# Kernel tuning notes

Hardware: AMD Instinct MI355X
Metric: run time of the kernel (lower is better)

The kernel has to match this reference:

```python
import jax, jax.numpy as jnp
import numpy as np

DS_DIM = 2
N_EXPERTS = 64
N_CLASSES = 26
IMG = 68
BATCH = 8192
FLAT = 1960  # 10 * 14 * 14 after two conv+pool stages


def _conv2d(x, w, b):
    # x: [B, Cin, H, W], w: [Cout, Cin, kh, kw]
    y = jax.lax.conv_general_dilated(
        x, w, window_strides=(1, 1), padding='VALID',
        dimension_numbers=('NCHW', 'OIHW', 'NCHW'))
    return y + b[None, :, None, None]


def _maxpool2(x):
    return jax.lax.reduce_window(
        x, -jnp.inf, jax.lax.max,
        window_dimensions=(1, 1, 2, 2), window_strides=(1, 1, 2, 2),
        padding='VALID')


def setup_inputs() -> dict:
    key = jax.random.key(0)
    ks = jax.random.split(key, 14)
    x = jax.random.normal(ks[0], (BATCH, DS_DIM), dtype=jnp.float32)
    cls_idx = jax.random.randint(ks[1], (BATCH,), 0, N_CLASSES)
    images = jax.random.normal(ks[2], (N_CLASSES, 1, IMG, IMG), dtype=jnp.float32)
    s = 0.05
    conv1_w = jax.random.normal(ks[3], (5, 1, 5, 5), dtype=jnp.float32) * s
    conv1_b = jax.random.normal(ks[4], (5,), dtype=jnp.float32) * s
    conv2_w = jax.random.normal(ks[5], (10, 5, 5, 5), dtype=jnp.float32) * s
    conv2_b = jax.random.normal(ks[6], (10,), dtype=jnp.float32) * s
    fc1_w = jax.random.normal(ks[7], (500, FLAT + DS_DIM), dtype=jnp.float32) * s
    fc1_b = jax.random.normal(ks[8], (500,), dtype=jnp.float32) * s
    fc2_w = jax.random.normal(ks[9], (N_EXPERTS, 500), dtype=jnp.float32) * s
    fc2_b = jax.random.normal(ks[10], (N_EXPERTS,), dtype=jnp.float32) * s
    # geotorch-constrained expert matrices: B_A positive-semidefinite, C_A skew
    raw_b = jax.random.normal(ks[11], (N_EXPERTS, DS_DIM, DS_DIM), dtype=jnp.float32)
    A_B = jnp.einsum('nik,njk->nij', raw_b, raw_b) * 0.1        # PSD
    raw_c = jax.random.normal(ks[12], (N_EXPERTS, DS_DIM, DS_DIM), dtype=jnp.float32)
    A_C = (raw_c - jnp.swapaxes(raw_c, -1, -2)) * 0.5            # skew
    x_tar = jax.random.normal(ks[13], (1, DS_DIM), dtype=jnp.float32)
    return {'x': x, 'cls_idx': cls_idx, 'images': images,
            'conv1_w': conv1_w, 'conv1_b': conv1_b,
            'conv2_w': conv2_w, 'conv2_b': conv2_b,
            'fc1_w': fc1_w, 'fc1_b': fc1_b,
            'fc2_w': fc2_w, 'fc2_b': fc2_b,
            'A_B': A_B, 'A_C': A_C, 'x_tar': x_tar}


def reference(x, cls_idx, images, conv1_w, conv1_b, conv2_w, conv2_b,
              fc1_w, fc1_b, fc2_w, fc2_b, A_B, A_C, x_tar):
    # gating CNN: gather per-sample image by class index
    img = images[cls_idx]                             # [B, 1, 68, 68]
    h = _maxpool2(jax.nn.relu(_conv2d(img, conv1_w, conv1_b)))   # [B, 5, 32, 32]
    h = _maxpool2(jax.nn.relu(_conv2d(h, conv2_w, conv2_b)))     # [B, 10, 14, 14]
    h = h.reshape(h.shape[0], -1)                     # [B, 1960]
    h = jnp.concatenate([h, x], axis=1)               # [B, 1962]
    h = jax.nn.relu(h @ fc1_w.T + fc1_b)              # [B, 500]
    w_all = jax.nn.softmax(h @ fc2_w.T + fc2_b, axis=1)  # [B, N]
    # fused expert weighted-sum (original: python loop over N tiny matmuls)
    A = A_B + A_C                                     # [N, d, d]
    diff = x_tar - x                                  # [B, d]
    s_all = jnp.einsum('bn,nij,bj->bi', w_all, A, diff)
    return s_all
```

## Files before the change

### kernel.cpp

```cpp
#include <hip/hip_runtime.h>

#define WS_SC1    0
#define WS_FEAT   133120
#define WS_FC1P   184080
#define WS_W2     197080
#define WS_AFLAT  229848
#define WS_WX     230104

__global__ __launch_bounds__(256) void k_conv1(
    const float* __restrict__ images, const float* __restrict__ c1w,
    const float* __restrict__ c1b, const float* __restrict__ fc2w,
    const float* __restrict__ fc1w, const float* __restrict__ A_B,
    const float* __restrict__ A_C, float* __restrict__ ws)
{
    const int b = blockIdx.x, t = threadIdx.x;
    if (b >= 520) {
        if (b == 520) {
            float* W2 = ws + WS_W2;
            for (int i = t; i < 32000; i += 256) {
                int k = i >> 6, e = i & 63;
                W2[i] = fc2w[e * 500 + k];
            }
        } else {
            float* Af = ws + WS_AFLAT;
            if (t < 256) Af[t] = A_B[t] + A_C[t];
            float* Wx = ws + WS_WX;
            for (int i = t; i < 1000; i += 256) {
                int j = i >> 1, k = i & 1;
                Wx[i] = fc1w[j * 1962 + 1960 + k];
            }
        }
        return;
    }

    const int c = b / 20, r = b - c * 20;
    const int oc = r >> 2, g = r & 3;
    const int py = g * 8 + (t >> 5), px = t & 31;

    float wr[25];
#pragma unroll
    for (int i = 0; i < 25; ++i) wr[i] = c1w[oc * 25 + i];
    const float bias = c1b[oc];

    const float* im = images + c * 4624 + (2 * py) * 68 + 2 * px;
    float ir[6][6];
#pragma unroll
    for (int a = 0; a < 6; ++a)
#pragma unroll
        for (int q = 0; q < 3; ++q) {
            float2 v = *(const float2*)&im[a * 68 + 2 * q];
            ir[a][2 * q] = v.x; ir[a][2 * q + 1] = v.y;
        }

    float a00 = bias, a01 = bias, a10 = bias, a11 = bias;
#pragma unroll
    for (int ky = 0; ky < 5; ++ky)
#pragma unroll
        for (int kx = 0; kx < 5; ++kx) {
            float w = wr[ky * 5 + kx];
            a00 += w * ir[ky][kx];     a01 += w * ir[ky][kx + 1];
            a10 += w * ir[ky + 1][kx]; a11 += w * ir[ky + 1][kx + 1];
        }
    float v = fmaxf(fmaxf(fmaxf(a00, a01), fmaxf(a10, a11)), 0.f);
    ws[WS_SC1 + ((c * 5 + oc) * 32 + py) * 32 + px] = v;
}

__global__ __launch_bounds__(256) void k_conv2(
    const float* __restrict__ c2w, const float* __restrict__ c2b,
    float* __restrict__ ws)
{
    const int b = blockIdx.x, t = threadIdx.x;
    const int c = b / 10, oc = b - c * 10;

    __shared__ float sw[125];
    if (t < 125) sw[t] = c2w[oc * 125 + t];
    __syncthreads();
    if (t >= 196) return;

    const int py = t / 14, px = t - py * 14;
    const float bias = c2b[oc];
    float a00 = bias, a01 = bias, a10 = bias, a11 = bias;

    const float* base = ws + WS_SC1 + c * 5120 + (2 * py) * 32 + 2 * px;
#pragma unroll
    for (int ic = 0; ic < 5; ++ic) {
        const float* s1 = base + ic * 1024;
        float ir[6][6];
#pragma unroll
        for (int a = 0; a < 6; ++a)
#pragma unroll
            for (int q = 0; q < 3; ++q) {
                float2 v = *(const float2*)&s1[a * 32 + 2 * q];
                ir[a][2 * q] = v.x; ir[a][2 * q + 1] = v.y;
            }
#pragma unroll
        for (int ky = 0; ky < 5; ++ky)
#pragma unroll
            for (int kx = 0; kx < 5; ++kx) {
                float w = sw[ic * 25 + ky * 5 + kx];
                a00 += w * ir[ky][kx];     a01 += w * ir[ky][kx + 1];
                a10 += w * ir[ky + 1][kx]; a11 += w * ir[ky + 1][kx + 1];
            }
    }
    float v = fmaxf(fmaxf(fmaxf(a00, a01), fmaxf(a10, a11)), 0.f);
    ws[WS_FEAT + c * 1960 + oc * 196 + py * 14 + px] = v;
}

__global__ __launch_bounds__(256) void k_fc1(
    const float* __restrict__ fc1w, const float* __restrict__ fc1b,
    float* __restrict__ ws)
{
    const int lane = threadIdx.x & 63, w = threadIdx.x >> 6;
    const int c = blockIdx.x / 63, jg = blockIdx.x - c * 63;
    const int j0 = jg * 8 + 2 * w;
    if (j0 >= 500) return;
    const int j1 = j0 + 1;

    const float* f  = ws + WS_FEAT + c * 1960;
    const float* w0 = fc1w + j0 * 1962;
    const float* w1 = fc1w + j1 * 1962;

    float acc0 = 0.f, acc1 = 0.f;
#pragma unroll
    for (int i = 0; i < 30; ++i) {
        int k = lane + 64 * i;
        float fv = f[k];
        acc0 += w0[k] * fv;
        acc1 += w1[k] * fv;
    }
    {
        int k = lane + 1920;
        if (k < 1960) {
            float fv = f[k];
            acc0 += w0[k] * fv;
            acc1 += w1[k] * fv;
        }
    }
#pragma unroll
    for (int off = 32; off >= 1; off >>= 1) {
        acc0 += __shfl_xor(acc0, off);
        acc1 += __shfl_xor(acc1, off);
    }
    if (lane == 0) {
        ws[WS_FC1P + c * 500 + j0] = acc0 + fc1b[j0];
        ws[WS_FC1P + c * 500 + j1] = acc1 + fc1b[j1];
    }
}

__global__ __launch_bounds__(512) void k_logits(
    const float* __restrict__ x, const int* __restrict__ cls,
    const float* __restrict__ fc2b, const float* __restrict__ x_tar,
    const float* __restrict__ ws, float* __restrict__ out)
{
    __shared__ float hs[32 * 501];
    __shared__ float lg[2 * 32 * 64];
    const int t = threadIdx.x;
    const int b0 = blockIdx.x * 32;
    const float* fc1p = ws + WS_FC1P;
    const float* Wx   = ws + WS_WX;
    const float* W2   = ws + WS_W2;
    const float* Af   = ws + WS_AFLAT;

    {
        const int sl = t >> 4;
        const int j0 = t & 15;
        const int b  = b0 + sl;
        const int c  = cls[b];
        const float x0 = x[2 * b], x1 = x[2 * b + 1];
        const float* fr = fc1p + c * 500;
        float* hr = hs + sl * 501;
        for (int j = j0; j < 500; j += 16) {
            float2 wx = *(const float2*)&Wx[2 * j];
            hr[j] = fmaxf(fr[j] + x0 * wx.x + x1 * wx.y, 0.f);
        }
    }
    __syncthreads();

    {
        const int kh = t >> 8;
        const int r  = t & 255;
        const int s0 = (r & 15) * 2;
        const int e0 = (r >> 4) * 4;
        const float* h0p = hs + s0 * 501;
        const float* h1p = h0p + 501;
        float4 a0 = make_float4(0.f, 0.f, 0.f, 0.f);
        float4 a1 = make_float4(0.f, 0.f, 0.f, 0.f);
        const int kbeg = kh * 250, kend = kbeg + 250;
#pragma unroll 5
        for (int k = kbeg; k < kend; ++k) {
            float hv0 = h0p[k], hv1 = h1p[k];
            float4 wv = *(const float4*)&W2[k * 64 + e0];
            a0.x += hv0 * wv.x; a0.y += hv0 * wv.y;
            a0.z += hv0 * wv.z; a0.w += hv0 * wv.w;
            a1.x += hv1 * wv.x; a1.y += hv1 * wv.y;
            a1.z += hv1 * wv.z; a1.w += hv1 * wv.w;
        }
        *(float4*)&lg[(kh * 32 + s0) * 64 + e0]     = a0;
        *(float4*)&lg[(kh * 32 + s0 + 1) * 64 + e0] = a1;
    }
    __syncthreads();

    {
        const int wv_ = t >> 6;
        const int e   = t & 63;
        const float xt0 = x_tar[0], xt1 = x_tar[1];
        const float be = fc2b[e];
        const float4 a4 = *(const float4*)&Af[4 * e];
#pragma unroll
        for (int i = 0; i < 4; ++i) {
            const int s = wv_ * 4 + i;
            float logit = be + lg[s * 64 + e] + lg[(32 + s) * 64 + e];
            float m = logit;
#pragma unroll
            for (int off = 32; off >= 1; off >>= 1) m = fmaxf(m, __shfl_xor(m, off));
            float ex = __expf(logit - m);
            float sum = ex;
            float m0 = ex * a4.x, m1 = ex * a4.y, m2 = ex * a4.z, m3 = ex * a4.w;
#pragma unroll
            for (int off = 32; off >= 1; off >>= 1) {
                sum += __shfl_xor(sum, off);
                m0 += __shfl_xor(m0, off);
                m1 += __shfl_xor(m1, off);
                m2 += __shfl_xor(m2, off);
                m3 += __shfl_xor(m3, off);
            }
            if (e == 0) {
                const int b = b0 + s;
                float d0 = xt0 - x[2 * b], d1 = xt1 - x[2 * b + 1];
                float inv = 1.f / sum;
                out[2 * b]     = (m0 * d0 + m1 * d1) * inv;
                out[2 * b + 1] = (m2 * d0 + m3 * d1) * inv;
            }
        }
    }
}

extern "C" void kernel_launch(void* const* d_in, const int* in_sizes, int n_in,
                              void* d_out, int out_size, void* d_ws, size_t ws_size,
                              hipStream_t stream) {
    const float* x      = (const float*)d_in[0];
    const int*   cls    = (const int*)  d_in[1];
    const float* images = (const float*)d_in[2];
    const float* c1w    = (const float*)d_in[3];
    const float* c1b    = (const float*)d_in[4];
    const float* c2w    = (const float*)d_in[5];
    const float* c2b    = (const float*)d_in[6];
    const float* fc1w   = (const float*)d_in[7];
    const float* fc1b   = (const float*)d_in[8];
    const float* fc2w   = (const float*)d_in[9];
    const float* fc2b   = (const float*)d_in[10];
    const float* A_B    = (const float*)d_in[11];
    const float* A_C    = (const float*)d_in[12];
    const float* x_tar  = (const float*)d_in[13];
    float* out = (float*)d_out;
    float* ws  = (float*)d_ws;

    k_conv1 <<<522, 256, 0, stream>>>(images, c1w, c1b, fc2w, fc1w, A_B, A_C, ws);
    k_conv2 <<<260, 256, 0, stream>>>(c2w, c2b, ws);
    k_fc1   <<<1638, 256, 0, stream>>>(fc1w, fc1b, ws);
    k_logits<<<256, 512, 0, stream>>>(x, cls, fc2b, x_tar, ws, out);
}
```

Measured before the change: 146.3 us.

## Fuse conv1 and conv2 in shared memory; register-tile the fc2 logits kernel

Merges the two convolution kernels into one. Each block loads its class image into LDS, recomputes all five conv1 channels there, then runs conv2 for one output channel. This removes a launch and the global round-trip for the conv1 activations, at the cost of computing conv1 ten times per class. The logits kernel now handles 16 samples per 256-thread block, splits K four ways and uses a 4x4 sample-by-expert register tile with float4 LDS reads. This gives more FMA reuse per load and more blocks.

```diff
diff --git a/kernel.cpp b/kernel.cpp
--- a/kernel.cpp
+++ b/kernel.cpp
@@ -1,21 +1,22 @@
 #include <hip/hip_runtime.h>
 
-#define WS_SC1    0
-#define WS_FEAT   133120
-#define WS_FC1P   184080
-#define WS_W2     197080
-#define WS_AFLAT  229848
-#define WS_WX     230104
-
-__global__ __launch_bounds__(256) void k_conv1(
-    const float* __restrict__ images, const float* __restrict__ c1w,
-    const float* __restrict__ c1b, const float* __restrict__ fc2w,
-    const float* __restrict__ fc1w, const float* __restrict__ A_B,
-    const float* __restrict__ A_C, float* __restrict__ ws)
+#define WS_FEAT   0
+#define WS_FC1P   50960
+#define WS_W2     63960
+#define WS_AFLAT  95960
+#define WS_WX     96216
+
+__global__ __launch_bounds__(256) void k_cnn(
+    const float* __restrict__ images,
+    const float* __restrict__ c1w, const float* __restrict__ c1b,
+    const float* __restrict__ c2w, const float* __restrict__ c2b,
+    const float* __restrict__ fc2w, const float* __restrict__ fc1w,
+    const float* __restrict__ A_B, const float* __restrict__ A_C,
+    float* __restrict__ ws)
 {
     const int b = blockIdx.x, t = threadIdx.x;
-    if (b >= 520) {
-        if (b == 520) {
+    if (b >= 260) {
+        if (b == 260) {
             float* W2 = ws + WS_W2;
             for (int i = t; i < 32000; i += 256) {
                 int k = i >> 6, e = i & 63;
@@ -33,77 +34,80 @@
         return;
     }
 
-    const int c = b / 20, r = b - c * 20;
-    const int oc = r >> 2, g = r & 3;
-    const int py = g * 8 + (t >> 5), px = t & 31;
-
-    float wr[25];
-#pragma unroll
-    for (int i = 0; i < 25; ++i) wr[i] = c1w[oc * 25 + i];
-    const float bias = c1b[oc];
-
-    const float* im = images + c * 4624 + (2 * py) * 68 + 2 * px;
-    float ir[6][6];
-#pragma unroll
-    for (int a = 0; a < 6; ++a)
-#pragma unroll
-        for (int q = 0; q < 3; ++q) {
-            float2 v = *(const float2*)&im[a * 68 + 2 * q];
-            ir[a][2 * q] = v.x; ir[a][2 * q + 1] = v.y;
-        }
-
-    float a00 = bias, a01 = bias, a10 = bias, a11 = bias;
-#pragma unroll
-    for (int ky = 0; ky < 5; ++ky)
-#pragma unroll
-        for (int kx = 0; kx < 5; ++kx) {
-            float w = wr[ky * 5 + kx];
-            a00 += w * ir[ky][kx];     a01 += w * ir[ky][kx + 1];
-            a10 += w * ir[ky + 1][kx]; a11 += w * ir[ky + 1][kx + 1];
-        }
-    float v = fmaxf(fmaxf(fmaxf(a00, a01), fmaxf(a10, a11)), 0.f);
-    ws[WS_SC1 + ((c * 5 + oc) * 32 + py) * 32 + px] = v;
-}
-
-__global__ __launch_bounds__(256) void k_conv2(
-    const float* __restrict__ c2w, const float* __restrict__ c2b,
-    float* __restrict__ ws)
-{
-    const int b = blockIdx.x, t = threadIdx.x;
     const int c = b / 10, oc = b - c * 10;
 
-    __shared__ float sw[125];
-    if (t < 125) sw[t] = c2w[oc * 125 + t];
-    __syncthreads();
-    if (t >= 196) return;
-
-    const int py = t / 14, px = t - py * 14;
-    const float bias = c2b[oc];
-    float a00 = bias, a01 = bias, a10 = bias, a11 = bias;
-
-    const float* base = ws + WS_SC1 + c * 5120 + (2 * py) * 32 + 2 * px;
-#pragma unroll
-    for (int ic = 0; ic < 5; ++ic) {
-        const float* s1 = base + ic * 1024;
+    __shared__ float simg[4624];
+    __shared__ float sc1[5 * 32 * 34];
+    __shared__ float sw1[125];
+    __shared__ float sb1[5];
+    __shared__ float sw2[125];
+
+    {
+        const float* im = images + c * 4624;
+        for (int i = t; i < 2312; i += 256)
+            *(float2*)&simg[2 * i] = *(const float2*)&im[2 * i];
+        for (int i = t; i < 125; i += 256) sw1[i] = c1w[i];
+        if (t < 5) sb1[t] = c1b[t];
+        for (int i = t; i < 125; i += 256) sw2[i] = c2w[oc * 125 + i];
+    }
+    __syncthreads();
+
+#pragma unroll
+    for (int r = 0; r < 4; ++r) {
+        const int pos = t + 256 * r;
+        const int py = pos >> 5, px = pos & 31;
         float ir[6][6];
 #pragma unroll
         for (int a = 0; a < 6; ++a)
 #pragma unroll
             for (int q = 0; q < 3; ++q) {
-                float2 v = *(const float2*)&s1[a * 32 + 2 * q];
+                float2 v = *(const float2*)&simg[(2 * py + a) * 68 + 2 * px + 2 * q];
                 ir[a][2 * q] = v.x; ir[a][2 * q + 1] = v.y;
             }
 #pragma unroll
-        for (int ky = 0; ky < 5; ++ky)
-#pragma unroll
-            for (int kx = 0; kx < 5; ++kx) {
-                float w = sw[ic * 25 + ky * 5 + kx];
-                a00 += w * ir[ky][kx];     a01 += w * ir[ky][kx + 1];
-                a10 += w * ir[ky + 1][kx]; a11 += w * ir[ky + 1][kx + 1];
-            }
-    }
-    float v = fmaxf(fmaxf(fmaxf(a00, a01), fmaxf(a10, a11)), 0.f);
-    ws[WS_FEAT + c * 1960 + oc * 196 + py * 14 + px] = v;
+        for (int o = 0; o < 5; ++o) {
+            float bias = sb1[o];
+            float a00 = bias, a01 = bias, a10 = bias, a11 = bias;
+#pragma unroll
+            for (int ky = 0; ky < 5; ++ky)
+#pragma unroll
+                for (int kx = 0; kx < 5; ++kx) {
+                    float w = sw1[o * 25 + ky * 5 + kx];
+                    a00 += w * ir[ky][kx];     a01 += w * ir[ky][kx + 1];
+                    a10 += w * ir[ky + 1][kx]; a11 += w * ir[ky + 1][kx + 1];
+                }
+            sc1[o * 1088 + py * 34 + px] =
+                fmaxf(fmaxf(fmaxf(a00, a01), fmaxf(a10, a11)), 0.f);
+        }
+    }
+    __syncthreads();
+
+    if (t < 196) {
+        const int py = t / 14, px = t - py * 14;
+        const float bias = c2b[oc];
+        float a00 = bias, a01 = bias, a10 = bias, a11 = bias;
+#pragma unroll
+        for (int ic = 0; ic < 5; ++ic) {
+            float ir[6][6];
+#pragma unroll
+            for (int a = 0; a < 6; ++a)
+#pragma unroll
+                for (int q = 0; q < 3; ++q) {
+                    float2 v = *(const float2*)&sc1[ic * 1088 + (2 * py + a) * 34 + 2 * px + 2 * q];
+                    ir[a][2 * q] = v.x; ir[a][2 * q + 1] = v.y;
+                }
+#pragma unroll
+            for (int ky = 0; ky < 5; ++ky)
+#pragma unroll
+                for (int kx = 0; kx < 5; ++kx) {
+                    float w = sw2[ic * 25 + ky * 5 + kx];
+                    a00 += w * ir[ky][kx];     a01 += w * ir[ky][kx + 1];
+                    a10 += w * ir[ky + 1][kx]; a11 += w * ir[ky + 1][kx + 1];
+                }
+        }
+        float v = fmaxf(fmaxf(fmaxf(a00, a01), fmaxf(a10, a11)), 0.f);
+        ws[WS_FEAT + c * 1960 + oc * 196 + py * 14 + px] = v;
+    }
 }
 
 __global__ __launch_bounds__(256) void k_fc1(
@@ -147,15 +151,15 @@
     }
 }
 
-__global__ __launch_bounds__(512) void k_logits(
+__global__ __launch_bounds__(256) void k_moe(
     const float* __restrict__ x, const int* __restrict__ cls,
     const float* __restrict__ fc2b, const float* __restrict__ x_tar,
     const float* __restrict__ ws, float* __restrict__ out)
 {
-    __shared__ float hs[32 * 501];
-    __shared__ float lg[2 * 32 * 64];
+    __shared__ float hs[16 * 508];
+    __shared__ float lg[4 * 16 * 64];
     const int t = threadIdx.x;
-    const int b0 = blockIdx.x * 32;
+    const int b0 = blockIdx.x * 16;
     const float* fc1p = ws + WS_FC1P;
     const float* Wx   = ws + WS_WX;
     const float* W2   = ws + WS_W2;
@@ -168,7 +172,7 @@
         const int c  = cls[b];
         const float x0 = x[2 * b], x1 = x[2 * b + 1];
         const float* fr = fc1p + c * 500;
-        float* hr = hs + sl * 501;
+        float* hr = hs + sl * 508;
         for (int j = j0; j < 500; j += 16) {
             float2 wx = *(const float2*)&Wx[2 * j];
             hr[j] = fmaxf(fr[j] + x0 * wx.x + x1 * wx.y, 0.f);
@@ -177,26 +181,50 @@
     __syncthreads();
 
     {
-        const int kh = t >> 8;
-        const int r  = t & 255;
-        const int s0 = (r & 15) * 2;
-        const int e0 = (r >> 4) * 4;
-        const float* h0p = hs + s0 * 501;
-        const float* h1p = h0p + 501;
+        const int kq = __builtin_amdgcn_readfirstlane(t >> 6);
+        const int rr = t & 63;
+        const int e0 = (rr >> 2) * 4;
+        const int s0 = (rr & 3) * 4;
+        const int kbeg = kq * 128;
+        const int kcnt = (kq == 3) ? 116 : 128;
+
         float4 a0 = make_float4(0.f, 0.f, 0.f, 0.f);
-        float4 a1 = make_float4(0.f, 0.f, 0.f, 0.f);
-        const int kbeg = kh * 250, kend = kbeg + 250;
-#pragma unroll 5
-        for (int k = kbeg; k < kend; ++k) {
-            float hv0 = h0p[k], hv1 = h1p[k];
-            float4 wv = *(const float4*)&W2[k * 64 + e0];
-            a0.x += hv0 * wv.x; a0.y += hv0 * wv.y;
-            a0.z += hv0 * wv.z; a0.w += hv0 * wv.w;
-            a1.x += hv1 * wv.x; a1.y += hv1 * wv.y;
-            a1.z += hv1 * wv.z; a1.w += hv1 * wv.w;
-        }
-        *(float4*)&lg[(kh * 32 + s0) * 64 + e0]     = a0;
-        *(float4*)&lg[(kh * 32 + s0 + 1) * 64 + e0] = a1;
+        float4 a1 = a0, a2 = a0, a3 = a0;
+        const float* h0p = hs + (s0 + 0) * 508;
+        const float* h1p = hs + (s0 + 1) * 508;
+        const float* h2p = hs + (s0 + 2) * 508;
+        const float* h3p = hs + (s0 + 3) * 508;
+
+        for (int k = kbeg; k < kbeg + kcnt; k += 4) {
+            float4 w0 = *(const float4*)&W2[(k + 0) * 64 + e0];
+            float4 w1 = *(const float4*)&W2[(k + 1) * 64 + e0];
+            float4 w2 = *(const float4*)&W2[(k + 2) * 64 + e0];
+            float4 w3 = *(const float4*)&W2[(k + 3) * 64 + e0];
+            float4 h0 = *(const float4*)&h0p[k];
+            float4 h1 = *(const float4*)&h1p[k];
+            float4 h2 = *(const float4*)&h2p[k];
+            float4 h3 = *(const float4*)&h3p[k];
+            a0.x += h0.x*w0.x + h0.y*w1.x + h0.z*w2.x + h0.w*w3.x;
+            a0.y += h0.x*w0.y + h0.y*w1.y + h0.z*w2.y + h0.w*w3.y;
+            a0.z += h0.x*w0.z + h0.y*w1.z + h0.z*w2.z + h0.w*w3.z;
+            a0.w += h0.x*w0.w + h0.y*w1.w + h0.z*w2.w + h0.w*w3.w;
+            a1.x += h1.x*w0.x + h1.y*w1.x + h1.z*w2.x + h1.w*w3.x;
+            a1.y += h1.x*w0.y + h1.y*w1.y + h1.z*w2.y + h1.w*w3.y;
+            a1.z += h1.x*w0.z + h1.y*w1.z + h1.z*w2.z + h1.w*w3.z;
+            a1.w += h1.x*w0.w + h1.y*w1.w + h1.z*w2.w + h1.w*w3.w;
+            a2.x += h2.x*w0.x + h2.y*w1.x + h2.z*w2.x + h2.w*w3.x;
+            a2.y += h2.x*w0.y + h2.y*w1.y + h2.z*w2.y + h2.w*w3.y;
+            a2.z += h2.x*w0.z + h2.y*w1.z + h2.z*w2.z + h2.w*w3.z;
+            a2.w += h2.x*w0.w + h2.y*w1.w + h2.z*w2.w + h2.w*w3.w;
+            a3.x += h3.x*w0.x + h3.y*w1.x + h3.z*w2.x + h3.w*w3.x;
+            a3.y += h3.x*w0.y + h3.y*w1.y + h3.z*w2.y + h3.w*w3.y;
+            a3.z += h3.x*w0.z + h3.y*w1.z + h3.z*w2.z + h3.w*w3.z;
+            a3.w += h3.x*w0.w + h3.y*w1.w + h3.z*w2.w + h3.w*w3.w;
+        }
+        *(float4*)&lg[(kq * 16 + s0 + 0) * 64 + e0] = a0;
+        *(float4*)&lg[(kq * 16 + s0 + 1) * 64 + e0] = a1;
+        *(float4*)&lg[(kq * 16 + s0 + 2) * 64 + e0] = a2;
+        *(float4*)&lg[(kq * 16 + s0 + 3) * 64 + e0] = a3;
     }
     __syncthreads();
 
@@ -209,7 +237,8 @@
 #pragma unroll
         for (int i = 0; i < 4; ++i) {
             const int s = wv_ * 4 + i;
-            float logit = be + lg[s * 64 + e] + lg[(32 + s) * 64 + e];
+            float logit = be + lg[s * 64 + e] + lg[(16 + s) * 64 + e]
+                        + lg[(32 + s) * 64 + e] + lg[(48 + s) * 64 + e];
             float m = logit;
 #pragma unroll
             for (int off = 32; off >= 1; off >>= 1) m = fmaxf(m, __shfl_xor(m, off));
@@ -255,8 +284,8 @@
     float* out = (float*)d_out;
     float* ws  = (float*)d_ws;
 
-    k_conv1 <<<522, 256, 0, stream>>>(images, c1w, c1b, fc2w, fc1w, A_B, A_C, ws);
-    k_conv2 <<<260, 256, 0, stream>>>(c2w, c2b, ws);
-    k_fc1   <<<1638, 256, 0, stream>>>(fc1w, fc1b, ws);
-    k_logits<<<256, 512, 0, stream>>>(x, cls, fc2b, x_tar, ws, out);
-}
+    k_cnn<<<262, 256, 0, stream>>>(images, c1w, c1b, c2w, c2b, fc2w, fc1w,
+                                   A_B, A_C, ws);
+    k_fc1<<<1638, 256, 0, stream>>>(fc1w, fc1b, ws);
+    k_moe<<<512, 256, 0, stream>>>(x, cls, fc2b, x_tar, ws, out);
+}
```

Result: no change. 145.4 us (-0.6%).
